# Optimization experiments

Hardware: AMD Instinct MI355X
Metric: run time of the kernel (lower is better)

## Reference

```python
import jax, jax.numpy as jnp
import numpy as np

EPS = 1e-5
N_HEADS = 16
D_NOPE = 128
D_ROPE = 64
D_QK = D_NOPE + D_ROPE  # 192
D_V = 128
KV_RANK = 512
SCALE = D_QK ** -0.5


def rms_norm(x, w, eps=EPS):
    return x * jax.lax.rsqrt(jnp.mean(x * x, axis=-1, keepdims=True) + eps) * w


def apply_rope(x, c, s):
    # x: [..., D_ROPE], c/s broadcastable [..., D_ROPE//2]; half-split rotation
    x0, x1 = x[..., : D_ROPE // 2], x[..., D_ROPE // 2 :]
    return jnp.concatenate([x0 * c - x1 * s, x0 * s + x1 * c], axis=-1)


def setup_inputs() -> dict:
    key = jax.random.key(0)
    ks = jax.random.split(key, 8)
    B, S, H_DIM = 2, 2048, 2048
    Q_RANK = 1536
    w = lambda k, shp: jax.random.normal(k, shp, dtype=jnp.float32) * 0.02
    # real RoPE tables: [max_seq, D_ROPE//2]
    inv_freq = 1.0 / (10000.0 ** (np.arange(0, D_ROPE, 2, dtype=np.float32) / D_ROPE))
    ang = np.arange(S, dtype=np.float32)[:, None] * inv_freq[None, :]
    return {
        "x": jax.random.normal(ks[0], (B, S, H_DIM), dtype=jnp.float32),
        "positions": jnp.arange(S, dtype=jnp.int64),
        "Wqa": w(ks[1], (H_DIM, Q_RANK)),
        "g_qa": jnp.ones((Q_RANK,), jnp.float32),
        "Wqb": w(ks[2], (Q_RANK, N_HEADS * D_QK)),
        "Wkva": w(ks[3], (H_DIM, KV_RANK + D_ROPE)),
        "g_kva": jnp.ones((KV_RANK,), jnp.float32),
        "Wkvb": w(ks[4], (KV_RANK, N_HEADS * (D_NOPE + D_V))),
        "Wo": w(ks[5], (N_HEADS * D_V, H_DIM)),
        "cos": jnp.asarray(np.cos(ang)),
        "sin": jnp.asarray(np.sin(ang)),
    }


def reference(x, positions, Wqa, g_qa, Wqb, Wkva, g_kva, Wkvb, Wo, cos, sin):
    B, S, _ = x.shape
    # Q path: low-rank down, RMSNorm, up
    q = rms_norm(x @ Wqa, g_qa) @ Wqb  # [B,S,H*D_QK]
    q = q.reshape(B, S, N_HEADS, D_QK)
    q_nope, q_rope = q[..., :D_NOPE], q[..., D_NOPE:]
    c = cos[positions]  # [S, D_ROPE//2]
    s = sin[positions]
    q_rope = apply_rope(q_rope, c[None, :, None, :], s[None, :, None, :])
    # KV path: joint down-proj, split latent / rope-key
    kv_a = x @ Wkva  # [B,S,KV_RANK+D_ROPE]
    kv_latent = rms_norm(kv_a[..., :KV_RANK], g_kva)
    k_rope = apply_rope(kv_a[..., KV_RANK:], c[None, :, :], s[None, :, :])  # [B,S,D_ROPE]
    # up-project latent to per-head k_nope and v
    kv_b = (kv_latent @ Wkvb).reshape(B, S, N_HEADS, D_NOPE + D_V)
    k_nope, v = kv_b[..., :D_NOPE], kv_b[..., D_NOPE:]
    k = jnp.concatenate(
        [k_nope, jnp.broadcast_to(k_rope[:, :, None, :], (B, S, N_HEADS, D_ROPE))], axis=-1
    )  # [B,S,H,D_QK]
    q_full = jnp.concatenate([q_nope, q_rope], axis=-1)  # [B,S,H,D_QK]
    # causal SDPA with d_qk != d_v
    scores = jnp.einsum("bqhd,bkhd->bhqk", q_full, k) * SCALE
    causal = jnp.tril(jnp.ones((S, S), dtype=bool))
    scores = jnp.where(causal[None, None, :, :], scores, -jnp.inf)
    p = jax.nn.softmax(scores, axis=-1)
    out = jnp.einsum("bhqk,bkhd->bqhd", p, v).reshape(B, S, N_HEADS * D_V)
    return out @ Wo
```

## Files before the change

kernel.cpp:

```cpp
#include <hip/hip_runtime.h>
#include <hip/hip_bf16.h>

typedef __bf16 bf16;
typedef __bf16 bf16x8 __attribute__((ext_vector_type(8)));
typedef __bf16 bf16x4 __attribute__((ext_vector_type(4)));
typedef float f32x4 __attribute__((ext_vector_type(4)));

#define B_    2
#define S_    2048
#define HD    2048
#define NH    16
#define DQK   192
#define DV    128
#define QR    1536
#define KVR   512
#define NTOK  4096
#define NKVB  4096
#define NQB   3072
#define NQKVAP 2304

#define EXP2F(x) __builtin_amdgcn_exp2f(x)

static __device__ __forceinline__ void gload16(const void* g, void* l) {
  __builtin_amdgcn_global_load_lds(
      (const __attribute__((address_space(1))) void*)g,
      (__attribute__((address_space(3))) void*)l, 16, 0, 0);
}

struct TransArgs {
  const float *s0, *s1, *s2, *s3, *s4, *x;
  bf16 *d0, *d1, *d2, *d3, *d4, *xb;
};
__global__ __launch_bounds__(256) void transpose_all(TransArgs a) {
  __shared__ float tile[32][33];
  int bid = blockIdx.x;
  if (bid >= 15360) {
    long i = ((long)(bid - 15360) * 256 + threadIdx.x) * 4;
    float4 v = *(const float4*)(a.x + i);
    bf16x4 o = {(bf16)v.x, (bf16)v.y, (bf16)v.z, (bf16)v.w};
    *(bf16x4*)(a.xb + i) = o;
    return;
  }
  int seg, rel;
  if      (bid < 3072)  { seg = 0; rel = bid; }
  else if (bid < 4608)  { seg = 1; rel = bid - 3072; }
  else if (bid < 9216)  { seg = 2; rel = bid - 4608; }
  else if (bid < 11264) { seg = 3; rel = bid - 9216; }
  else                  { seg = 4; rel = bid - 11264; }
  const float* in = seg == 0 ? a.s0 : seg == 1 ? a.s1 : seg == 2 ? a.s2 : seg == 3 ? a.s3 : a.s4;
  bf16* out       = seg == 0 ? a.d0 : seg == 1 ? a.d1 : seg == 2 ? a.d2 : seg == 3 ? a.d3 : a.d4;
  int R   = seg == 0 ? 2048 : seg == 1 ? 2048 : seg == 2 ? 1536 : seg == 3 ? 512 : 2048;
  int C   = seg == 0 ? 1536 : seg == 1 ? 576  : seg == 2 ? 3072 : seg == 3 ? 4096 : 2048;
  int Np  = seg == 0 ? 1536 : seg == 1 ? 768  : seg == 2 ? 3072 : seg == 3 ? 4096 : 2048;
  int nbx = seg == 0 ? 48   : seg == 1 ? 24   : seg == 2 ? 96   : seg == 3 ? 128 : 64;
  int c0 = (rel % nbx) * 32;
  int r0 = (rel / nbx) * 32;
  int tx = threadIdx.x & 31, ty = threadIdx.x >> 5;
#pragma unroll
  for (int i = 0; i < 4; ++i) {
    int r = r0 + ty + i * 8, c = c0 + tx;
    tile[ty + i * 8][tx] = (c < C) ? in[(long)r * C + c] : 0.f;
  }
  __syncthreads();
#pragma unroll
  for (int i = 0; i < 4; ++i) {
    int oc = c0 + ty + i * 8;
    if (oc < Np) out[(long)oc * R + r0 + tx] = (bf16)tile[tx][ty + i * 8];
  }
}

#define GEMM_CORE(A, Bt, K)                                                    \
  __shared__ bf16 As[128 * 64];                                                \
  __shared__ bf16 Bs[128 * 64];                                                \
  const int t = threadIdx.x;                                                   \
  const int l = t & 63;                                                        \
  const int w = t >> 6;                                                        \
  const int m0 = blockIdx.y * 128;                                             \
  const int n0 = blockIdx.x * 128;                                             \
  const int wr = (w >> 1) * 64;                                                \
  const int wc = (w & 1) * 64;                                                 \
  const int lr = l & 15;                                                       \
  const int lg = l >> 4;                                                       \
  f32x4 acc[4][4] = {};                                                        \
  for (int k0 = 0; k0 < (K); k0 += 64) {                                       \
    __syncthreads();                                                           \
    _Pragma("unroll")                                                          \
    for (int j = 0; j < 4; ++j) {                                              \
      int s = j * 256 + t;                                                     \
      int row = s >> 3, sc = s & 7;                                            \
      int c = sc ^ (row & 7);                                                  \
      gload16((A) + (long)(m0 + row) * (K) + k0 + c * 8,                       \
              As + (j * 256 + w * 64) * 8);                                    \
      gload16((Bt) + (long)(n0 + row) * (K) + k0 + c * 8,                      \
              Bs + (j * 256 + w * 64) * 8);                                    \
    }                                                                          \
    __syncthreads();                                                           \
    _Pragma("unroll")                                                          \
    for (int kh = 0; kh < 2; ++kh) {                                           \
      bf16x8 af[4], bfr[4];                                                    \
      _Pragma("unroll")                                                        \
      for (int m = 0; m < 4; ++m) {                                            \
        int row = wr + m * 16 + lr;                                            \
        af[m] = *(const bf16x8*)(As + row * 64 + (((kh * 4 + lg) ^ (row & 7)) << 3)); \
      }                                                                        \
      _Pragma("unroll")                                                        \
      for (int n = 0; n < 4; ++n) {                                            \
        int row = wc + n * 16 + lr;                                            \
        bfr[n] = *(const bf16x8*)(Bs + row * 64 + (((kh * 4 + lg) ^ (row & 7)) << 3)); \
      }                                                                        \
      _Pragma("unroll")                                                        \
      for (int m = 0; m < 4; ++m)                                              \
        _Pragma("unroll")                                                      \
        for (int n = 0; n < 4; ++n)                                            \
          acc[m][n] = __builtin_amdgcn_mfma_f32_16x16x32_bf16(af[m], bfr[n], acc[m][n], 0, 0, 0); \
    }                                                                          \
  }

template <typename CT>
__global__ __launch_bounds__(256) void gemm_bf16(const bf16* __restrict__ A,
                                                 const bf16* __restrict__ Bt,
                                                 CT* __restrict__ C,
                                                 int M, int N, int K) {
  GEMM_CORE(A, Bt, K)
#pragma unroll
  for (int m = 0; m < 4; ++m)
#pragma unroll
    for (int n = 0; n < 4; ++n)
#pragma unroll
      for (int v = 0; v < 4; ++v) {
        int row = m0 + wr + m * 16 + lg * 4 + v;
        int col = n0 + wc + n * 16 + lr;
        C[(long)row * N + col] = (CT)acc[m][n][v];
      }
}

#define G8P_BODY(A, Bt, K, M0, N0)                                             \
  const int t = threadIdx.x;                                                   \
  const int w = t >> 6, l = t & 63;                                            \
  const int lr = l & 15, lg = l >> 4;                                          \
  const int wm = w >> 2, wn = w & 3;                                           \
  const int m0 = (M0), n0 = (N0);                                              \
  const int NT = (K) >> 6;                                                     \
  const int tr = t >> 3, sc = t & 7;                                           \
  f32x4 acc[8][4] = {};                                                        \
  auto stg = [&](int kt, int j) {                                              \
    int jj = j & 3;                                                            \
    int row = jj * 64 + tr;                                                    \
    int c = sc ^ (row & 7);                                                    \
    const bf16* src = (j < 4)                                                  \
        ? (A)  + (long)(m0 + row) * (K) + kt * 64 + c * 8                      \
        : (Bt) + (long)(n0 + row) * (K) + kt * 64 + c * 8;                     \
    bf16* dst = ((j < 4) ? As_[kt & 1] : Bs_[kt & 1]) + (jj * 512 + w * 64) * 8; \
    gload16(src, dst);                                                         \
  };                                                                           \
  _Pragma("unroll") for (int j = 0; j < 8; ++j) stg(0, j);                     \
  _Pragma("unroll") for (int j = 0; j < 8; ++j) stg(1, j);                     \
  for (int kt = 0; kt < NT; ++kt) {                                            \
    const bf16* Ab = As_[kt & 1];                                              \
    const bf16* Bb = Bs_[kt & 1];                                              \
    if (kt == NT - 1) { asm volatile("s_waitcnt vmcnt(0)" ::: "memory"); }     \
    else              { asm volatile("s_waitcnt vmcnt(8)" ::: "memory"); }     \
    __builtin_amdgcn_s_barrier();                                              \
    asm volatile("" ::: "memory");                                             \
    bf16x8 af[8][2], bfr[4][2];                                                \
    _Pragma("unroll")                                                          \
    for (int mi = 0; mi < 8; ++mi) {                                           \
      int row = wm * 128 + mi * 16 + lr;                                       \
      _Pragma("unroll")                                                        \
      for (int kh = 0; kh < 2; ++kh)                                           \
        af[mi][kh] = *(const bf16x8*)(Ab + row * 64 + (((kh * 4 + lg) ^ (row & 7)) << 3)); \
    }                                                                          \
    _Pragma("unroll")                                                          \
    for (int ni = 0; ni < 4; ++ni) {                                           \
      int row = wn * 64 + ni * 16 + lr;                                        \
      _Pragma("unroll")                                                        \
      for (int kh = 0; kh < 2; ++kh)                                           \
        bfr[ni][kh] = *(const bf16x8*)(Bb + row * 64 + (((kh * 4 + lg) ^ (row & 7)) << 3)); \
    }                                                                          \
    asm volatile("s_waitcnt lgkmcnt(0)" ::: "memory");                         \
    __builtin_amdgcn_sched_barrier(0);                                         \
    __builtin_amdgcn_s_setprio(1);                                             \
    _Pragma("unroll")                                                          \
    for (int mi = 0; mi < 8; ++mi)                                             \
      _Pragma("unroll")                                                        \
      for (int kh = 0; kh < 2; ++kh)                                           \
        acc[mi][0] = __builtin_amdgcn_mfma_f32_16x16x32_bf16(af[mi][kh], bfr[0][kh], acc[mi][0], 0, 0, 0); \
    __builtin_amdgcn_s_setprio(0);                                             \
    __builtin_amdgcn_s_barrier();    \
    asm volatile("" ::: "memory");                                             \
    bool more = (kt + 2) < NT;                                                 \
    if (more) { stg(kt + 2, 0); stg(kt + 2, 1); stg(kt + 2, 2); }              \
    __builtin_amdgcn_s_setprio(1);                                             \
    _Pragma("unroll")                                                          \
    for (int mi = 0; mi < 8; ++mi)                                             \
      _Pragma("unroll")                                                        \
      for (int kh = 0; kh < 2; ++kh)                                           \
        acc[mi][1] = __builtin_amdgcn_mfma_f32_16x16x32_bf16(af[mi][kh], bfr[1][kh], acc[mi][1], 0, 0, 0); \
    __builtin_amdgcn_s_setprio(0);                                             \
    if (more) { stg(kt + 2, 3); stg(kt + 2, 4); stg(kt + 2, 5); }              \
    __builtin_amdgcn_s_setprio(1);                                             \
    _Pragma("unroll")                                                          \
    for (int mi = 0; mi < 8; ++mi)                                             \
      _Pragma("unroll")                                                        \
      for (int kh = 0; kh < 2; ++kh)                                           \
        acc[mi][2] = __builtin_amdgcn_mfma_f32_16x16x32_bf16(af[mi][kh], bfr[2][kh], acc[mi][2], 0, 0, 0); \
    __builtin_amdgcn_s_setprio(0);                                             \
    if (more) { stg(kt + 2, 6); stg(kt + 2, 7); }                              \
    __builtin_amdgcn_s_setprio(1);                                             \
    _Pragma("unroll")                                                          \
    for (int mi = 0; mi < 8; ++mi)                                             \
      _Pragma("unroll")                                                        \
      for (int kh = 0; kh < 2; ++kh)                                           \
        acc[mi][3] = __builtin_amdgcn_mfma_f32_16x16x32_bf16(af[mi][kh], bfr[3][kh], acc[mi][3], 0, 0, 0); \
    __builtin_amdgcn_s_setprio(0);                                             \
  }

template <typename CT>
__global__ __launch_bounds__(512) void gemm8p_c(const bf16* __restrict__ A,
                                                const bf16* __restrict__ Bt,
                                                CT* __restrict__ C,
                                                int N, int K) {
  __shared__ bf16 As_[2][256 * 64];
  __shared__ bf16 Bs_[2][256 * 64];
  G8P_BODY(A, Bt, K, blockIdx.y * 256, blockIdx.x * 256)
#pragma unroll
  for (int mi = 0; mi < 8; ++mi)
#pragma unroll
    for (int ni = 0; ni < 4; ++ni)
#pragma unroll
      for (int v = 0; v < 4; ++v) {
        int row = m0 + wm * 128 + mi * 16 + lg * 4 + v;
        int col = n0 + wn * 64 + ni * 16 + lr;
        C[(long)row * N + col] = (CT)acc[mi][ni][v];
      }
}

__global__ __launch_bounds__(512) void gemm8p_qkv(
    const bf16* __restrict__ q_n,  const bf16* __restrict__ Wqb_t,
    const bf16* __restrict__ kv_l, const bf16* __restrict__ Wkvb_t,
    const int* __restrict__ pos,
    const float* __restrict__ cosT, const float* __restrict__ sinT,
    bf16* __restrict__ q_bhsd, bf16* __restrict__ k_bhsd,
    bf16* __restrict__ v_t) {
  __shared__ bf16 As_[2][256 * 64];
  __shared__ bf16 Bs_[2][256 * 64];
  int bid = blockIdx.x;
  if (bid < 192) {
    const float SCALE = 0.07216878364870323f * 1.4426950408889634f;
    int bx = bid % 12, by = bid / 12;
    G8P_BODY(q_n, Wqb_t, QR, by * 256, bx * 256)
    int c0 = n0 + wn * 64;
    int h = c0 / 192;
    int part = c0 - h * 192;
#pragma unroll
    for (int mi = 0; mi < 8; ++mi)
#pragma unroll
      for (int v = 0; v < 4; ++v) {
        int row = m0 + wm * 128 + mi * 16 + lg * 4 + v;
        int b = row >> 11, s = row & (S_ - 1);
        long base = ((long)(b * NH + h) * S_ + s) * DQK;
        if (part < 128) {
#pragma unroll
          for (int ni = 0; ni < 4; ++ni)
            q_bhsd[base + part + ni * 16 + lr] = (bf16)(acc[mi][ni][v] * SCALE);
        } else {
          int p = pos[s] & (S_ - 1);
          float c_lo = cosT[p * 32 + lr],      s_lo = sinT[p * 32 + lr];
          float c_hi = cosT[p * 32 + 16 + lr], s_hi = sinT[p * 32 + 16 + lr];
          float o0 = acc[mi][0][v] * c_lo - acc[mi][2][v] * s_lo;
          float o1 = acc[mi][1][v] * c_hi - acc[mi][3][v] * s_hi;
          float o2 = acc[mi][0][v] * s_lo + acc[mi][2][v] * c_lo;
          float o3 = acc[mi][1][v] * s_hi + acc[mi][3][v] * c_hi;
          q_bhsd[base + 128 + lr] = (bf16)(o0 * SCALE);
          q_bhsd[base + 144 + lr] = (bf16)(o1 * SCALE);
          q_bhsd[base + 160 + lr] = (bf16)(o2 * SCALE);
          q_bhsd[base + 176 + lr] = (bf16)(o3 * SCALE);
        }
      }
  } else {
    int rel = bid - 192;
    int bx = rel & 15, by = rel >> 4;
    G8P_BODY(kv_l, Wkvb_t, KVR, by * 256, bx * 256)
    int c0 = n0 + wn * 64;
    int h = c0 >> 8;
    int dbase = c0 & 64;
    bool vpart = (c0 >> 7) & 1;
    if (!vpart) {
#pragma unroll
      for (int mi = 0; mi < 8; ++mi)
#pragma unroll
        for (int v = 0; v < 4; ++v) {
          int row = m0 + wm * 128 + mi * 16 + lg * 4 + v;
          int b = row >> 11, s = row & (S_ - 1);
          long base = ((long)(b * NH + h) * S_ + s) * DQK + dbase;
#pragma unroll
          for (int ni = 0; ni < 4; ++ni)
            k_bhsd[base + ni * 16 + lr] = (bf16)acc[mi][ni][v];
        }
    } else {
#pragma unroll
      for (int mi = 0; mi < 8; ++mi) {
        int row0 = m0 + wm * 128 + mi * 16 + lg * 4;
        int b = row0 >> 11, s = row0 & (S_ - 1);
#pragma unroll
        for (int ni = 0; ni < 4; ++ni) {
          int d = dbase + ni * 16 + lr;
          bf16x4 o = {(bf16)acc[mi][ni][0], (bf16)acc[mi][ni][1],
                      (bf16)acc[mi][ni][2], (bf16)acc[mi][ni][3]};
          *(bf16x4*)(v_t + ((long)(b * NH + h) * DV + d) * S_ + s) = o;
        }
      }
    }
  }
}

__global__ __launch_bounds__(256) void norm_prep(const bf16* __restrict__ xa,
                                                 const float* __restrict__ g_qa,
                                                 const float* __restrict__ g_kva,
                                                 const int* __restrict__ pos,
                                                 const float* __restrict__ cosT,
                                                 const float* __restrict__ sinT,
                                                 bf16* __restrict__ q_n,
                                                 bf16* __restrict__ kv_l,
                                                 bf16* __restrict__ k_bhsd) {
  int row = blockIdx.x;
  int t = threadIdx.x;
  int b = row >> 11, s = row & (S_ - 1);
  const bf16* xr = xa + (long)row * NQKVAP;
  __shared__ float red[3];
  __shared__ bf16 rope_s[64];
  float vf[8];
  if (t < 192) {
    bf16x8 vv = *(const bf16x8*)(xr + t * 8);
    float ss = 0.f;
#pragma unroll
    for (int e = 0; e < 8; ++e) { vf[e] = (float)vv[e]; ss += vf[e] * vf[e]; }
#pragma unroll
    for (int m = 1; m < 64; m <<= 1) ss += __shfl_xor(ss, m);
    if ((t & 63) == 0) red[t >> 6] = ss;
  } else {
    int tt = t - 192;
    const bf16* xl = xr + QR;
    bf16x8 vv = *(const bf16x8*)(xl + tt * 8);
    float ss = 0.f;
#pragma unroll
    for (int e = 0; e < 8; ++e) { vf[e] = (float)vv[e]; ss += vf[e] * vf[e]; }
#pragma unroll
    for (int m = 1; m < 64; m <<= 1) ss += __shfl_xor(ss, m);
    float rs = rsqrtf(ss / KVR + 1e-5f);
    bf16x8 o;
#pragma unroll
    for (int e = 0; e < 8; ++e) o[e] = (bf16)(vf[e] * rs * g_kva[tt * 8 + e]);
    *(bf16x8*)(kv_l + (long)row * KVR + tt * 8) = o;
    if (tt < 32) {
      int p = pos[s] & (S_ - 1);
      float c = cosT[p * 32 + tt], sn = sinT[p * 32 + tt];
      float x0 = (float)xl[512 + tt], x1 = (float)xl[544 + tt];
      rope_s[tt] = (bf16)(x0 * c - x1 * sn);
      rope_s[32 + tt] = (bf16)(x0 * sn + x1 * c);
    }
  }
  __syncthreads();
  if (t < 192) {
    float ss = red[0] + red[1] + red[2];
    float rs = rsqrtf(ss / QR + 1e-5f);
    bf16x8 o;
#pragma unroll
    for (int e = 0; e < 8; ++e) o[e] = (bf16)(vf[e] * rs * g_qa[t * 8 + e]);
    *(bf16x8*)(q_n + (long)row * QR + t * 8) = o;
  } else {
    int tt = t - 192;
    bf16x8 rv = *(const bf16x8*)&rope_s[(tt & 7) * 8];
    long base0 = ((long)(b * NH + (tt >> 3)) * S_ + s) * DQK + 128 + (tt & 7) * 8;
    long base1 = ((long)(b * NH + 8 + (tt >> 3)) * S_ + s) * DQK + 128 + (tt & 7) * 8;
    *(bf16x8*)(k_bhsd + base0) = rv;
    *(bf16x8*)(k_bhsd + base1) = rv;
  }
}

#define KVB  64
#define DVP  144
__global__ __launch_bounds__(512) void flash4(const bf16* __restrict__ q_bhsd,
                                              const bf16* __restrict__ k_bhsd,
                                              const bf16* __restrict__ v_t,
                                              bf16* __restrict__ att) {
  __shared__ bf16 Ks[KVB * DQK];
  __shared__ bf16 Vs[DVP * KVB];
  __shared__ bf16 Ps[8][16 * 72];
  int bid = blockIdx.x;
  int bh = bid & 31;
  int qt = 15 - (bid >> 5);
  int b = bh >> 4, h = bh & 15;
  int q0 = qt * 128;
  int t = threadIdx.x;
  int w = t >> 6, l = t & 63;
  int lr = l & 15, lg = l >> 4;
  int qw = q0 + w * 16;

  const bf16* Qb = q_bhsd + (long)bh * S_ * DQK;
  const bf16* Kb = k_bhsd + (long)bh * S_ * DQK;
  const bf16* Vb = v_t + (long)bh * DV * S_;

  if (t < 128) {
    int rr = 128 + (t >> 3), cc = (t & 7) * 8;
    bf16 val = (bf16)((rr == 128) ? 1.0f : 0.0f);
    bf16x8 vvv = {val, val, val, val, val, val, val, val};
    *(bf16x8*)(Vs + rr * KVB + cc) = vvv;
  }

  bf16x8 qf[6];
#pragma unroll
  for (int t6 = 0; t6 < 6; ++t6)
    qf[t6] = *(const bf16x8*)(Qb + (long)(qw + lr) * DQK + t6 * 32 + lg * 8);

  f32x4 oacc[9] = {};
  float mrow[4] = {-1e30f, -1e30f, -1e30f, -1e30f};
  const int lr7 = lr & 7;

  int nkt = 2 * qt + 2;
  for (int kt = 0; kt < nkt; ++kt) {
    int k0 = kt * KVB;
    __syncthreads();
#pragma unroll
    for (int j = 0; j < 3; ++j) {
      int s = j * 512 + t;
      int r = s / 24, c1 = s - r * 24;
      int c = c1 ^ (r & 7);
      gload16(Kb + (long)(k0 + r) * DQK + c * 8, Ks + (j * 512 + w * 64) * 8);
    }
#pragma unroll
    for (int j = 0; j < 2; ++j) {
      int s = j * 512 + t;
      int d = s >> 3, c1 = s & 7;
      int c = c1 ^ (d & 7);
      gload16(Vb + (long)d * S_ + k0 + c * 8, Vs + (j * 512 + w * 64) * 8);
    }
    __syncthreads();
    if (k0 > qw + 15) continue;

    f32x4 sacc[4] = {};
#pragma unroll
    for (int n = 0; n < 4; ++n) {
      int rk = n * 16 + lr;
#pragma unroll
      for (int t6 = 0; t6 < 6; ++t6) {
        bf16x8 kf = *(const bf16x8*)(Ks + rk * DQK + (((t6 * 4 + lg) ^ lr7) << 3));
        sacc[n] = __builtin_amdgcn_mfma_f32_16x16x32_bf16(qf[t6], kf, sacc[n], 0, 0, 0);
      }
    }
    if (k0 + KVB - 1 > qw) {
#pragma unroll
      for (int n = 0; n < 4; ++n)
#pragma unroll
        for (int v = 0; v < 4; ++v) {
          int r = lg * 4 + v, c = n * 16 + lr;
          if (k0 + c > qw + r) sacc[n][v] = -1e30f;
        }
    }
    float mv[4];
#pragma unroll
    for (int v = 0; v < 4; ++v) {
      mv[v] = fmaxf(fmaxf(sacc[0][v], sacc[1][v]), fmaxf(sacc[2][v], sacc[3][v]));
#pragma unroll
      for (int msk = 1; msk < 16; msk <<= 1) mv[v] = fmaxf(mv[v], __shfl_xor(mv[v], msk));
    }
    bool grow = (mv[0] > mrow[0] + 8.f) | (mv[1] > mrow[1] + 8.f) |
                (mv[2] > mrow[2] + 8.f) | (mv[3] > mrow[3] + 8.f);
    if (__any(grow)) {
      float corr[4];
#pragma unroll
      for (int v = 0; v < 4; ++v) {
        float mt = fmaxf(mrow[v], mv[v]);
        corr[v] = EXP2F(mrow[v] - mt);
        mrow[v] = mt;
      }
#pragma unroll
      for (int dn = 0; dn < 9; ++dn)
#pragma unroll
        for (int v = 0; v < 4; ++v) oacc[dn][v] *= corr[v];
    }
#pragma unroll
    for (int v = 0; v < 4; ++v)
#pragma unroll
      for (int n = 0; n < 4; ++n)
        Ps[w][(lg * 4 + v) * 72 + n * 16 + lr] = (bf16)EXP2F(sacc[n][v] - mrow[v]);
#pragma unroll
    for (int kc = 0; kc < 2; ++kc) {
      bf16x8 pf = *(const bf16x8*)(Ps[w] + lr * 72 + kc * 32 + lg * 8);
#pragma unroll
      for (int dn = 0; dn < 9; ++dn) {
        int d = dn * 16 + lr;
        bf16x8 vf = *(const bf16x8*)(Vs + d * KVB + (((kc * 4 + lg) ^ lr7) << 3));
        oacc[dn] = __builtin_amdgcn_mfma_f32_16x16x32_bf16(pf, vf, oacc[dn], 0, 0, 0);
      }
    }
  }
  float rl[4];
#pragma unroll
  for (int v = 0; v < 4; ++v) {
    float lv = __shfl(oacc[8][v], lg * 16);
    rl[v] = 1.0f / lv;
  }
#pragma unroll
  for (int dn = 0; dn < 8; ++dn)
#pragma unroll
    for (int v = 0; v < 4; ++v) {
      int r = lg * 4 + v;
      float o = oacc[dn][v] * rl[v];
      att[((long)(b * S_ + qw + r)) * 2048 + h * 128 + dn * 16 + lr] = (bf16)o;
    }
}

extern "C" void kernel_launch(void* const* d_in, const int* in_sizes, int n_in,
                              void* d_out, int out_size, void* d_ws, size_t ws_size,
                              hipStream_t stream) {
  const float* x        = (const float*)d_in[0];
  const int* pos        = (const int*)d_in[1];
  const float* Wqa      = (const float*)d_in[2];
  const float* g_qa     = (const float*)d_in[3];
  const float* Wqb      = (const float*)d_in[4];
  const float* Wkva     = (const float*)d_in[5];
  const float* g_kva    = (const float*)d_in[6];
  const float* Wkvb     = (const float*)d_in[7];
  const float* Wo       = (const float*)d_in[8];
  const float* cosT     = (const float*)d_in[9];
  const float* sinT     = (const float*)d_in[10];
  float* out            = (float*)d_out;

  size_t off = 0;
  char* wsp = (char*)d_ws;
  auto alloc = [&](size_t n) { void* p = wsp + off; off += (n + 255) & ~(size_t)255; return p; };
  bf16*  Wqa_t  = (bf16*) alloc((size_t)QR * HD * 2);
  bf16*  Wkva_t = (bf16*) alloc((size_t)768 * HD * 2);
  bf16*  Wqb_t  = (bf16*) alloc((size_t)NQB * QR * 2);
  bf16*  Wkvb_t = (bf16*) alloc((size_t)NKVB * KVR * 2);
  bf16*  Wo_t   = (bf16*) alloc((size_t)HD * HD * 2);
  bf16*  x_bf   = (bf16*) alloc((size_t)NTOK * HD * 2);
  bf16*  q_bhsd = (bf16*) alloc((size_t)B_ * NH * S_ * DQK * 2);
  bf16*  k_bhsd = (bf16*) alloc((size_t)B_ * NH * S_ * DQK * 2);
  bf16*  v_t    = (bf16*) alloc((size_t)B_ * NH * DV * S_ * 2);
  bf16*  att    = (bf16*) alloc((size_t)NTOK * 2048 * 2);
  char*  T      = (char*) alloc((size_t)37748736);
  bf16*  xa  = (bf16*)T;
  bf16*  q_n = (bf16*)(T + 18874368);
  bf16*  kv_l = (bf16*)(T + 18874368 + 12582912);
  if (ws_size < off) return;

  TransArgs ta = {Wqa, Wkva, Wqb, Wkvb, Wo, x,
                  Wqa_t, Wkva_t, Wqb_t, Wkvb_t, Wo_t, x_bf};
  transpose_all<<<23552, 256, 0, stream>>>(ta);
  gemm8p_c<bf16><<<dim3(NQKVAP / 256, NTOK / 256), 512, 0, stream>>>(x_bf, Wqa_t, xa, NQKVAP, HD);
  norm_prep<<<NTOK, 256, 0, stream>>>(xa, g_qa, g_kva, pos, cosT, sinT, q_n, kv_l, k_bhsd);
  gemm8p_qkv<<<448, 512, 0, stream>>>(q_n, Wqb_t, kv_l, Wkvb_t, pos, cosT, sinT,
                                      q_bhsd, k_bhsd, v_t);
  flash4<<<512, 512, 0, stream>>>(q_bhsd, k_bhsd, v_t, att);
  gemm_bf16<float><<<dim3(HD / 128, NTOK / 128), 256, 0, stream>>>(att, Wo_t, out, NTOK, HD, HD);
}
```

Measured before the change: 296.8 us.

## Overlap late-weight transposes with the first down-projection GEMM in one launch

The single transpose kernel is split. The first launch now converts x and transposes only Wqa/Wkva. The transposes of Wqb, Wkvb and Wo are folded into the first GEMM launch as extra blocks that run alongside the 144 GEMM tiles, so memory-bound transpose work can fill the GPU while the compute-bound GEMM runs. The risk is that transpose blocks carry the GEMM's large LDS footprint and 512-thread shape, which may limit occupancy. Block scheduling order may also delay the GEMM tiles.

```diff
diff --git a/kernel.cpp b/kernel.cpp
--- a/kernel.cpp
+++ b/kernel.cpp
@@ -27,32 +27,29 @@
       (__attribute__((address_space(3))) void*)l, 16, 0, 0);
 }
 
-struct TransArgs {
-  const float *s0, *s1, *s2, *s3, *s4, *x;
-  bf16 *d0, *d1, *d2, *d3, *d4, *xb;
+struct PrepArgs {
+  const float *x, *Wqa, *Wkva;
+  bf16 *xb, *Wqa_t, *Wkva_t;
 };
-__global__ __launch_bounds__(256) void transpose_all(TransArgs a) {
-  __shared__ float tile[32][33];
+__global__ __launch_bounds__(256) void prep_a(PrepArgs a) {
   int bid = blockIdx.x;
-  if (bid >= 15360) {
-    long i = ((long)(bid - 15360) * 256 + threadIdx.x) * 4;
+  if (bid < 8192) {
+    long i = ((long)bid * 256 + threadIdx.x) * 4;
     float4 v = *(const float4*)(a.x + i);
     bf16x4 o = {(bf16)v.x, (bf16)v.y, (bf16)v.z, (bf16)v.w};
     *(bf16x4*)(a.xb + i) = o;
     return;
   }
-  int seg, rel;
-  if      (bid < 3072)  { seg = 0; rel = bid; }
-  else if (bid < 4608)  { seg = 1; rel = bid - 3072; }
-  else if (bid < 9216)  { seg = 2; rel = bid - 4608; }
-  else if (bid < 11264) { seg = 3; rel = bid - 9216; }
-  else                  { seg = 4; rel = bid - 11264; }
-  const float* in = seg == 0 ? a.s0 : seg == 1 ? a.s1 : seg == 2 ? a.s2 : seg == 3 ? a.s3 : a.s4;
-  bf16* out       = seg == 0 ? a.d0 : seg == 1 ? a.d1 : seg == 2 ? a.d2 : seg == 3 ? a.d3 : a.d4;
-  int R   = seg == 0 ? 2048 : seg == 1 ? 2048 : seg == 2 ? 1536 : seg == 3 ? 512 : 2048;
-  int C   = seg == 0 ? 1536 : seg == 1 ? 576  : seg == 2 ? 3072 : seg == 3 ? 4096 : 2048;
-  int Np  = seg == 0 ? 1536 : seg == 1 ? 768  : seg == 2 ? 3072 : seg == 3 ? 4096 : 2048;
-  int nbx = seg == 0 ? 48   : seg == 1 ? 24   : seg == 2 ? 96   : seg == 3 ? 128 : 64;
+  __shared__ float tile[32][33];
+  int g = bid - 8192;
+  int seg = (g < 3072) ? 0 : 1;
+  int rel = (seg == 0) ? g : g - 3072;
+  const float* in = seg == 0 ? a.Wqa : a.Wkva;
+  bf16* out       = seg == 0 ? a.Wqa_t : a.Wkva_t;
+  int C   = seg == 0 ? 1536 : 576;
+  int Np  = seg == 0 ? 1536 : 768;
+  int nbx = seg == 0 ? 48 : 24;
+  const int R = 2048;
   int c0 = (rel % nbx) * 32;
   int r0 = (rel / nbx) * 32;
   int tx = threadIdx.x & 31, ty = threadIdx.x >> 5;
@@ -215,24 +212,60 @@
     __builtin_amdgcn_s_setprio(0);                                             \
   }
 
-template <typename CT>
-__global__ __launch_bounds__(512) void gemm8p_c(const bf16* __restrict__ A,
-                                                const bf16* __restrict__ Bt,
-                                                CT* __restrict__ C,
-                                                int N, int K) {
+struct XtArgs {
+  const bf16 *x_bf, *Wt;
+  bf16 *xa;
+  const float *Wqb, *Wkvb, *Wo;
+  bf16 *Wqb_t, *Wkvb_t, *Wo_t;
+};
+__global__ __launch_bounds__(512) void gemm8p_xt(XtArgs a) {
   __shared__ bf16 As_[2][256 * 64];
   __shared__ bf16 Bs_[2][256 * 64];
-  G8P_BODY(A, Bt, K, blockIdx.y * 256, blockIdx.x * 256)
-#pragma unroll
-  for (int mi = 0; mi < 8; ++mi)
-#pragma unroll
-    for (int ni = 0; ni < 4; ++ni)
-#pragma unroll
-      for (int v = 0; v < 4; ++v) {
-        int row = m0 + wm * 128 + mi * 16 + lg * 4 + v;
-        int col = n0 + wn * 64 + ni * 16 + lr;
-        C[(long)row * N + col] = (CT)acc[mi][ni][v];
-      }
+  __shared__ float ttile[2][32][33];
+  int bid = blockIdx.x;
+  if (bid >= 144) {
+    int half = threadIdx.x >> 8;
+    int tt = threadIdx.x & 255;
+    int g = (bid - 144) * 2 + half;
+    int seg, rel;
+    if      (g < 4608) { seg = 0; rel = g; }
+    else if (g < 6656) { seg = 1; rel = g - 4608; }
+    else               { seg = 2; rel = g - 6656; }
+    const float* in = seg == 0 ? a.Wqb : seg == 1 ? a.Wkvb : a.Wo;
+    bf16* out       = seg == 0 ? a.Wqb_t : seg == 1 ? a.Wkvb_t : a.Wo_t;
+    int R   = seg == 0 ? 1536 : seg == 1 ? 512 : 2048;
+    int C   = seg == 0 ? 3072 : seg == 1 ? 4096 : 2048;
+    int nbx = seg == 0 ? 96 : seg == 1 ? 128 : 64;
+    int c0 = (rel % nbx) * 32;
+    int r0 = (rel / nbx) * 32;
+    int tx = tt & 31, ty = tt >> 5;
+#pragma unroll
+    for (int i = 0; i < 4; ++i) {
+      int r = r0 + ty + i * 8, c = c0 + tx;
+      ttile[half][ty + i * 8][tx] = in[(long)r * C + c];
+    }
+    __syncthreads();
+#pragma unroll
+    for (int i = 0; i < 4; ++i) {
+      int oc = c0 + ty + i * 8;
+      out[(long)oc * R + r0 + tx] = (bf16)ttile[half][tx][ty + i * 8];
+    }
+    return;
+  }
+  {
+    int bx = bid % 9, by = bid / 9;
+    G8P_BODY(a.x_bf, a.Wt, HD, by * 256, bx * 256)
+#pragma unroll
+    for (int mi = 0; mi < 8; ++mi)
+#pragma unroll
+      for (int ni = 0; ni < 4; ++ni)
+#pragma unroll
+        for (int v = 0; v < 4; ++v) {
+          int row = m0 + wm * 128 + mi * 16 + lg * 4 + v;
+          int col = n0 + wn * 64 + ni * 16 + lr;
+          a.xa[(long)row * NQKVAP + col] = (bf16)acc[mi][ni][v];
+        }
+  }
 }
 
 __global__ __launch_bounds__(512) void gemm8p_qkv(
@@ -546,10 +579,10 @@
   bf16*  kv_l = (bf16*)(T + 18874368 + 12582912);
   if (ws_size < off) return;
 
-  TransArgs ta = {Wqa, Wkva, Wqb, Wkvb, Wo, x,
-                  Wqa_t, Wkva_t, Wqb_t, Wkvb_t, Wo_t, x_bf};
-  transpose_all<<<23552, 256, 0, stream>>>(ta);
-  gemm8p_c<bf16><<<dim3(NQKVAP / 256, NTOK / 256), 512, 0, stream>>>(x_bf, Wqa_t, xa, NQKVAP, HD);
+  PrepArgs pa = {x, Wqa, Wkva, x_bf, Wqa_t, Wkva_t};
+  prep_a<<<12800, 256, 0, stream>>>(pa);
+  XtArgs xt = {x_bf, Wqa_t, xa, Wqb, Wkvb, Wo, Wqb_t, Wkvb_t, Wo_t};
+  gemm8p_xt<<<5520, 512, 0, stream>>>(xt);
   norm_prep<<<NTOK, 256, 0, stream>>>(xa, g_qa, g_kva, pos, cosT, sinT, q_n, kv_l, k_bhsd);
   gemm8p_qkv<<<448, 512, 0, stream>>>(q_n, Wqb_t, kv_l, Wkvb_t, pos, cosT, sinT,
                                       q_bhsd, k_bhsd, v_t);
```

New measurement: 291.2 us (median of 2 runs). About the same (-1.9%).
